# Performance work log

Measured on AMD Instinct MI355X. Metric: run time of the kernel, lower is better.

## Reference

```python
import jax, jax.numpy as jnp
import numpy as np

N_STREAMS = 8192
ITERS = 5
EPS = 1e-6


def setup_inputs() -> dict:
    key = jax.random.key(0)
    # matches torch init: randn(n, n) * 0.1
    logits = jax.random.normal(key, (N_STREAMS, N_STREAMS), dtype=jnp.float32) * 0.1
    return {"logits": logits}


def reference(logits) -> jnp.ndarray:
    n = logits.shape[0]
    # M = sigmoid(logits) + I
    M = jax.nn.sigmoid(logits) + jnp.eye(n, dtype=logits.dtype)
    for _ in range(ITERS):
        M = M / (jnp.sum(M, axis=1, keepdims=True) + EPS)  # row normalize
        M = M / (jnp.sum(M, axis=0, keepdims=True) + EPS)  # col normalize
    return M
```

## Files before the change

kernel.cpp:

```cpp
#include <hip/hip_runtime.h>

#define N_DIM 8192
#define EPS 1e-6f
#define R_STRIP 16
#define NRB (N_DIM / R_STRIP)

__device__ __forceinline__ float bflo(unsigned u) { return __uint_as_float(u << 16); }
__device__ __forceinline__ float bfhi(unsigned u) { return __uint_as_float(u & 0xffff0000u); }
__device__ __forceinline__ unsigned f2bf_bits(float f) {
    unsigned u = __float_as_uint(f);
    return (u + 0x7fffu + ((u >> 16) & 1u)) >> 16;
}
__device__ __forceinline__ float sigmoidf_fast(float x) {
    return 1.f / (1.f + __expf(-x));
}
__device__ __forceinline__ float dot8(uint4 b, float4 c0, float4 c1) {
    return bflo(b.x) * c0.x + bfhi(b.x) * c0.y + bflo(b.y) * c0.z + bfhi(b.y) * c0.w
         + bflo(b.z) * c1.x + bfhi(b.z) * c1.y + bflo(b.w) * c1.z + bfhi(b.w) * c1.w;
}
__device__ __forceinline__ void acc8(float* a, uint4 b, float rr) {
    a[0] += bflo(b.x) * rr; a[1] += bfhi(b.x) * rr;
    a[2] += bflo(b.y) * rr; a[3] += bfhi(b.y) * rr;
    a[4] += bflo(b.z) * rr; a[5] += bfhi(b.z) * rr;
    a[6] += bflo(b.w) * rr; a[7] += bfhi(b.w) * rr;
}
__device__ __forceinline__ uint4 sig_pack8(float4 x0, float4 x1, int jbase, int row, float& t) {
    float s[8] = { sigmoidf_fast(x0.x), sigmoidf_fast(x0.y), sigmoidf_fast(x0.z), sigmoidf_fast(x0.w),
                   sigmoidf_fast(x1.x), sigmoidf_fast(x1.y), sigmoidf_fast(x1.z), sigmoidf_fast(x1.w) };
    #pragma unroll
    for (int k = 0; k < 8; ++k)
        if (jbase + k == row) s[k] += 1.f;
    unsigned b[8];
    #pragma unroll
    for (int k = 0; k < 8; ++k) {
        b[k] = f2bf_bits(s[k]);
        t += __uint_as_float(b[k] << 16);
    }
    return make_uint4(b[0] | (b[1] << 16), b[2] | (b[3] << 16),
                      b[4] | (b[5] << 16), b[6] | (b[7] << 16));
}

__global__ __launch_bounds__(256) void k_init(const float* __restrict__ logits,
                                              unsigned short* __restrict__ B,
                                              float* __restrict__ r,
                                              float* __restrict__ partial) {
    __shared__ float sred[2][4];
    const int tid = threadIdx.x;
    const int lane = tid & 63, wid = tid >> 6;
    const int i0 = blockIdx.x * R_STRIP;
    float a[4][8];
    #pragma unroll
    for (int s = 0; s < 4; ++s)
        #pragma unroll
        for (int k = 0; k < 8; ++k) a[s][k] = 0.f;

    for (int bb = 0; bb < R_STRIP / 2; ++bb) {
        const int row0 = i0 + 2 * bb, row1 = row0 + 1;
        const float4* l0 = (const float4*)(logits + (size_t)row0 * N_DIM);
        const float4* l1 = (const float4*)(logits + (size_t)row1 * N_DIM);
        uint4* w0 = (uint4*)(B + (size_t)row0 * N_DIM);
        uint4* w1 = (uint4*)(B + (size_t)row1 * N_DIM);
        uint4 b0[4], b1[4];
        float t0 = 0.f, t1 = 0.f;
        #pragma unroll
        for (int s = 0; s < 4; ++s) {
            const int v = s * 256 + tid;
            b0[s] = sig_pack8(l0[2 * v], l0[2 * v + 1], v * 8, row0, t0);
            b1[s] = sig_pack8(l1[2 * v], l1[2 * v + 1], v * 8, row1, t1);
            w0[v] = b0[s];
            w1[v] = b1[s];
        }
        #pragma unroll
        for (int off = 32; off > 0; off >>= 1) {
            t0 += __shfl_down(t0, off, 64);
            t1 += __shfl_down(t1, off, 64);
        }
        if (lane == 0) { sred[0][wid] = t0; sred[1][wid] = t1; }
        __syncthreads();
        const float T0 = sred[0][0] + sred[0][1] + sred[0][2] + sred[0][3];
        const float T1 = sred[1][0] + sred[1][1] + sred[1][2] + sred[1][3];
        const float r0 = 1.f / (T0 + EPS);
        const float r1 = 1.f / (T1 + EPS);
        __syncthreads();
        if (tid == 0) { r[row0] = r0; r[row1] = r1; }
        #pragma unroll
        for (int s = 0; s < 4; ++s) { acc8(a[s], b0[s], r0); acc8(a[s], b1[s], r1); }
    }
    float* p = partial + (size_t)blockIdx.x * N_DIM;
    #pragma unroll
    for (int s = 0; s < 4; ++s) {
        const int col = s * 2048 + tid * 8;
        *(float4*)(p + col)     = make_float4(a[s][0], a[s][1], a[s][2], a[s][3]);
        *(float4*)(p + col + 4) = make_float4(a[s][4], a[s][5], a[s][6], a[s][7]);
    }
}

__global__ __launch_bounds__(256) void k_fused(const unsigned short* __restrict__ B,
                                               const float* __restrict__ cvec,
                                               float* __restrict__ r,
                                               float* __restrict__ partial) {
    __shared__ float sred[2][4];
    const int tid = threadIdx.x;
    const int lane = tid & 63, wid = tid >> 6;
    const int i0 = blockIdx.x * R_STRIP;
    const float4* cv = (const float4*)cvec;
    float a[4][8];
    #pragma unroll
    for (int s = 0; s < 4; ++s)
        #pragma unroll
        for (int k = 0; k < 8; ++k) a[s][k] = 0.f;

    for (int bb = 0; bb < R_STRIP / 2; ++bb) {
        const int row0 = i0 + 2 * bb, row1 = row0 + 1;
        const float r0old = r[row0];
        const float r1old = r[row1];
        const uint4* br0 = (const uint4*)(B + (size_t)row0 * N_DIM);
        const uint4* br1 = (const uint4*)(B + (size_t)row1 * N_DIM);
        uint4 b0[4], b1[4];
        float t0 = 0.f, t1 = 0.f;
        #pragma unroll
        for (int s = 0; s < 4; ++s) {
            const int v = s * 256 + tid;
            b0[s] = br0[v];
            b1[s] = br1[v];
            const float4 c0 = cv[2 * v];
            const float4 c1 = cv[2 * v + 1];
            t0 += dot8(b0[s], c0, c1);
            t1 += dot8(b1[s], c0, c1);
        }
        #pragma unroll
        for (int off = 32; off > 0; off >>= 1) {
            t0 += __shfl_down(t0, off, 64);
            t1 += __shfl_down(t1, off, 64);
        }
        if (lane == 0) { sred[0][wid] = t0; sred[1][wid] = t1; }
        __syncthreads();
        const float T0 = sred[0][0] + sred[0][1] + sred[0][2] + sred[0][3];
        const float T1 = sred[1][0] + sred[1][1] + sred[1][2] + sred[1][3];
        const float r0 = r0old / (r0old * T0 + EPS);
        const float r1 = r1old / (r1old * T1 + EPS);
        __syncthreads();
        if (tid == 0) { r[row0] = r0; r[row1] = r1; }
        #pragma unroll
        for (int s = 0; s < 4; ++s) { acc8(a[s], b0[s], r0); acc8(a[s], b1[s], r1); }
    }
    float* p = partial + (size_t)blockIdx.x * N_DIM;
    #pragma unroll
    for (int s = 0; s < 4; ++s) {
        const int col = s * 2048 + tid * 8;
        *(float4*)(p + col)     = make_float4(a[s][0], a[s][1], a[s][2], a[s][3]);
        *(float4*)(p + col + 4) = make_float4(a[s][4], a[s][5], a[s][6], a[s][7]);
    }
}

__global__ __launch_bounds__(256) void k_cupd(const float* __restrict__ partial,
                                              float* __restrict__ cvec, int first) {
    __shared__ float s[4][64];
    const int tc = threadIdx.x & 63;
    const int tg = threadIdx.x >> 6;
    const int j = blockIdx.x * 64 + tc;
    float u = 0.f;
    #pragma unroll 8
    for (int rb = tg * (NRB / 4); rb < (tg + 1) * (NRB / 4); ++rb)
        u += partial[(size_t)rb * N_DIM + j];
    s[tg][tc] = u;
    __syncthreads();
    if (threadIdx.x < 64) {
        const float tot = s[0][tc] + s[1][tc] + s[2][tc] + s[3][tc];
        const float cj = first ? 1.f : cvec[j];
        cvec[j] = cj / (cj * tot + EPS);
    }
}

__global__ __launch_bounds__(256) void k_out(const unsigned short* __restrict__ B,
                                             const float* __restrict__ r,
                                             const float* __restrict__ cvec,
                                             float* __restrict__ out) {
    const int row = blockIdx.x;
    const float ri = r[row];
    const uint4* brow = (const uint4*)(B + (size_t)row * N_DIM);
    const float4* cv = (const float4*)cvec;
    float* orow = out + (size_t)row * N_DIM;
    #pragma unroll
    for (int it = 0; it < 4; ++it) {
        const int v = it * 256 + (int)threadIdx.x;
        const uint4 b = brow[v];
        const float4 c0 = cv[2 * v];
        const float4 c1 = cv[2 * v + 1];
        *(float4*)(orow + v * 8)     = make_float4(bflo(b.x) * ri * c0.x, bfhi(b.x) * ri * c0.y,
                                                   bflo(b.y) * ri * c0.z, bfhi(b.y) * ri * c0.w);
        *(float4*)(orow + v * 8 + 4) = make_float4(bflo(b.z) * ri * c1.x, bfhi(b.z) * ri * c1.y,
                                                   bflo(b.w) * ri * c1.z, bfhi(b.w) * ri * c1.w);
    }
}

__global__ __launch_bounds__(256) void k_out_logits(const float* __restrict__ logits,
                                                    const float* __restrict__ r,
                                                    const float* __restrict__ cvec,
                                                    float* __restrict__ out) {
    const int row = blockIdx.x;
    const float ri = r[row];
    const float4* lrow = (const float4*)(logits + (size_t)row * N_DIM);
    const float4* cv = (const float4*)cvec;
    float4* orow = (float4*)(out + (size_t)row * N_DIM);
    #pragma unroll
    for (int it = 0; it < 8; ++it) {
        const int v = it * 256 + (int)threadIdx.x;
        const float4 x = lrow[v];
        const float4 cc = cv[v];
        const int j = v * 4;
        float s0 = sigmoidf_fast(x.x); if (j     == row) s0 += 1.f;
        float s1 = sigmoidf_fast(x.y); if (j + 1 == row) s1 += 1.f;
        float s2 = sigmoidf_fast(x.z); if (j + 2 == row) s2 += 1.f;
        float s3 = sigmoidf_fast(x.w); if (j + 3 == row) s3 += 1.f;
        orow[v] = make_float4(s0 * ri * cc.x, s1 * ri * cc.y, s2 * ri * cc.z, s3 * ri * cc.w);
    }
}

extern "C" void kernel_launch(void* const* d_in, const int* in_sizes, int n_in,
                              void* d_out, int out_size, void* d_ws, size_t ws_size,
                              hipStream_t stream) {
    const float* logits = (const float*)d_in[0];
    float* out = (float*)d_out;
    const size_t nn = (size_t)N_DIM * N_DIM;
    const size_t need = nn * 2 + (2 * N_DIM + (size_t)NRB * N_DIM) * 4;
    const bool use_ws = ws_size >= need + 256;
    float* wsf = (float*)d_ws;
    unsigned short* B;
    float *r, *cvec, *partial;
    if (use_ws) {
        B = (unsigned short*)wsf;
        r = wsf + nn / 2;
    } else {
        B = (unsigned short*)(out + nn / 2);
        r = wsf;
    }
    cvec = r + N_DIM;
    partial = cvec + N_DIM;

    const dim3 blk(256);
    k_init<<<dim3(NRB), blk, 0, stream>>>(logits, B, r, partial);
    k_cupd<<<dim3(128), blk, 0, stream>>>(partial, cvec, 1);
    for (int it = 1; it < 5; ++it) {
        k_fused<<<dim3(NRB), blk, 0, stream>>>(B, cvec, r, partial);
        k_cupd<<<dim3(128), blk, 0, stream>>>(partial, cvec, 0);
    }
    if (use_ws)
        k_out<<<dim3(N_DIM), blk, 0, stream>>>(B, r, cvec, out);
    else
        k_out_logits<<<dim3(N_DIM), blk, 0, stream>>>(logits, r, cvec, out);
}
```

Baseline: 637.2 us.

## Use 1024-thread blocks that load a whole 16-row strip at once

The init and fused row-strip kernels now use 1024 threads per block. Each thread owns one 8-column slice and loads all 16 rows of the strip up front, so the eight sequential two-row passes, each with two barriers, become one batched load, one batched 16-way reduction and two barriers per block. The c vector is loaded once per thread instead of once per row pair, and logits are read with nontemporal loads. In exchange each thread holds 16 uint4 values plus 16 partial sums in registers, which may limit occupancy under the 1024-thread launch bound.

```diff
diff --git a/kernel.cpp b/kernel.cpp
--- a/kernel.cpp
+++ b/kernel.cpp
@@ -4,6 +4,9 @@
 #define EPS 1e-6f
 #define R_STRIP 16
 #define NRB (N_DIM / R_STRIP)
+#define TPB 1024
+
+typedef float f32x4v __attribute__((ext_vector_type(4)));
 
 __device__ __forceinline__ float bflo(unsigned u) { return __uint_as_float(u << 16); }
 __device__ __forceinline__ float bfhi(unsigned u) { return __uint_as_float(u & 0xffff0000u); }
@@ -40,117 +43,103 @@
                       b[4] | (b[5] << 16), b[6] | (b[7] << 16));
 }
 
-__global__ __launch_bounds__(256) void k_init(const float* __restrict__ logits,
-                                              unsigned short* __restrict__ B,
-                                              float* __restrict__ r,
-                                              float* __restrict__ partial) {
-    __shared__ float sred[2][4];
+__global__ __launch_bounds__(TPB, 4) void k_init(const float* __restrict__ logits,
+                                                 unsigned short* __restrict__ B,
+                                                 float* __restrict__ r,
+                                                 float* __restrict__ partial) {
+    __shared__ float sredT[16][16];
+    __shared__ float rr[16];
     const int tid = threadIdx.x;
     const int lane = tid & 63, wid = tid >> 6;
     const int i0 = blockIdx.x * R_STRIP;
-    float a[4][8];
-    #pragma unroll
-    for (int s = 0; s < 4; ++s)
-        #pragma unroll
-        for (int k = 0; k < 8; ++k) a[s][k] = 0.f;
-
-    for (int bb = 0; bb < R_STRIP / 2; ++bb) {
-        const int row0 = i0 + 2 * bb, row1 = row0 + 1;
-        const float4* l0 = (const float4*)(logits + (size_t)row0 * N_DIM);
-        const float4* l1 = (const float4*)(logits + (size_t)row1 * N_DIM);
-        uint4* w0 = (uint4*)(B + (size_t)row0 * N_DIM);
-        uint4* w1 = (uint4*)(B + (size_t)row1 * N_DIM);
-        uint4 b0[4], b1[4];
-        float t0 = 0.f, t1 = 0.f;
-        #pragma unroll
-        for (int s = 0; s < 4; ++s) {
-            const int v = s * 256 + tid;
-            b0[s] = sig_pack8(l0[2 * v], l0[2 * v + 1], v * 8, row0, t0);
-            b1[s] = sig_pack8(l1[2 * v], l1[2 * v + 1], v * 8, row1, t1);
-            w0[v] = b0[s];
-            w1[v] = b1[s];
-        }
-        #pragma unroll
-        for (int off = 32; off > 0; off >>= 1) {
-            t0 += __shfl_down(t0, off, 64);
-            t1 += __shfl_down(t1, off, 64);
-        }
-        if (lane == 0) { sred[0][wid] = t0; sred[1][wid] = t1; }
-        __syncthreads();
-        const float T0 = sred[0][0] + sred[0][1] + sred[0][2] + sred[0][3];
-        const float T1 = sred[1][0] + sred[1][1] + sred[1][2] + sred[1][3];
-        const float r0 = 1.f / (T0 + EPS);
-        const float r1 = 1.f / (T1 + EPS);
-        __syncthreads();
-        if (tid == 0) { r[row0] = r0; r[row1] = r1; }
-        #pragma unroll
-        for (int s = 0; s < 4; ++s) { acc8(a[s], b0[s], r0); acc8(a[s], b1[s], r1); }
-    }
-    float* p = partial + (size_t)blockIdx.x * N_DIM;
-    #pragma unroll
-    for (int s = 0; s < 4; ++s) {
-        const int col = s * 2048 + tid * 8;
-        *(float4*)(p + col)     = make_float4(a[s][0], a[s][1], a[s][2], a[s][3]);
-        *(float4*)(p + col + 4) = make_float4(a[s][4], a[s][5], a[s][6], a[s][7]);
-    }
-}
-
-__global__ __launch_bounds__(256) void k_fused(const unsigned short* __restrict__ B,
-                                               const float* __restrict__ cvec,
-                                               float* __restrict__ r,
-                                               float* __restrict__ partial) {
-    __shared__ float sred[2][4];
+    uint4 b[16];
+    float t[16];
+    #pragma unroll
+    for (int q = 0; q < 16; ++q) {
+        const int row = i0 + q;
+        const f32x4v* l = (const f32x4v*)(logits + (size_t)row * N_DIM);
+        const f32x4v xa = __builtin_nontemporal_load(l + 2 * tid);
+        const f32x4v xb = __builtin_nontemporal_load(l + 2 * tid + 1);
+        float tl = 0.f;
+        b[q] = sig_pack8(make_float4(xa.x, xa.y, xa.z, xa.w),
+                         make_float4(xb.x, xb.y, xb.z, xb.w), tid * 8, row, tl);
+        t[q] = tl;
+        ((uint4*)(B + (size_t)row * N_DIM))[tid] = b[q];
+    }
+    #pragma unroll
+    for (int off = 32; off > 0; off >>= 1)
+        #pragma unroll
+        for (int q = 0; q < 16; ++q) t[q] += __shfl_xor(t[q], off, 64);
+    if (lane == 0) {
+        #pragma unroll
+        for (int q = 0; q < 16; ++q) sredT[wid][q] = t[q];
+    }
+    __syncthreads();
+    if (tid < 16) {
+        float T = 0.f;
+        #pragma unroll
+        for (int w = 0; w < 16; ++w) T += sredT[w][tid];
+        const float rv = 1.f / (T + EPS);
+        rr[tid] = rv;
+        r[i0 + tid] = rv;
+    }
+    __syncthreads();
+    float a[8];
+    #pragma unroll
+    for (int k = 0; k < 8; ++k) a[k] = 0.f;
+    #pragma unroll
+    for (int q = 0; q < 16; ++q) acc8(a, b[q], rr[q]);
+    float* p = partial + (size_t)blockIdx.x * N_DIM + tid * 8;
+    *(float4*)p       = make_float4(a[0], a[1], a[2], a[3]);
+    *(float4*)(p + 4) = make_float4(a[4], a[5], a[6], a[7]);
+}
+
+__global__ __launch_bounds__(TPB, 4) void k_fused(const unsigned short* __restrict__ B,
+                                                  const float* __restrict__ cvec,
+                                                  float* __restrict__ r,
+                                                  float* __restrict__ partial) {
+    __shared__ float sredT[16][16];
+    __shared__ float rr[16];
     const int tid = threadIdx.x;
     const int lane = tid & 63, wid = tid >> 6;
     const int i0 = blockIdx.x * R_STRIP;
-    const float4* cv = (const float4*)cvec;
-    float a[4][8];
-    #pragma unroll
-    for (int s = 0; s < 4; ++s)
-        #pragma unroll
-        for (int k = 0; k < 8; ++k) a[s][k] = 0.f;
-
-    for (int bb = 0; bb < R_STRIP / 2; ++bb) {
-        const int row0 = i0 + 2 * bb, row1 = row0 + 1;
-        const float r0old = r[row0];
-        const float r1old = r[row1];
-        const uint4* br0 = (const uint4*)(B + (size_t)row0 * N_DIM);
-        const uint4* br1 = (const uint4*)(B + (size_t)row1 * N_DIM);
-        uint4 b0[4], b1[4];
-        float t0 = 0.f, t1 = 0.f;
-        #pragma unroll
-        for (int s = 0; s < 4; ++s) {
-            const int v = s * 256 + tid;
-            b0[s] = br0[v];
-            b1[s] = br1[v];
-            const float4 c0 = cv[2 * v];
-            const float4 c1 = cv[2 * v + 1];
-            t0 += dot8(b0[s], c0, c1);
-            t1 += dot8(b1[s], c0, c1);
-        }
-        #pragma unroll
-        for (int off = 32; off > 0; off >>= 1) {
-            t0 += __shfl_down(t0, off, 64);
-            t1 += __shfl_down(t1, off, 64);
-        }
-        if (lane == 0) { sred[0][wid] = t0; sred[1][wid] = t1; }
-        __syncthreads();
-        const float T0 = sred[0][0] + sred[0][1] + sred[0][2] + sred[0][3];
-        const float T1 = sred[1][0] + sred[1][1] + sred[1][2] + sred[1][3];
-        const float r0 = r0old / (r0old * T0 + EPS);
-        const float r1 = r1old / (r1old * T1 + EPS);
-        __syncthreads();
-        if (tid == 0) { r[row0] = r0; r[row1] = r1; }
-        #pragma unroll
-        for (int s = 0; s < 4; ++s) { acc8(a[s], b0[s], r0); acc8(a[s], b1[s], r1); }
-    }
-    float* p = partial + (size_t)blockIdx.x * N_DIM;
-    #pragma unroll
-    for (int s = 0; s < 4; ++s) {
-        const int col = s * 2048 + tid * 8;
-        *(float4*)(p + col)     = make_float4(a[s][0], a[s][1], a[s][2], a[s][3]);
-        *(float4*)(p + col + 4) = make_float4(a[s][4], a[s][5], a[s][6], a[s][7]);
-    }
+    const float4 c0 = ((const float4*)cvec)[2 * tid];
+    const float4 c1 = ((const float4*)cvec)[2 * tid + 1];
+    const uint4* bp = (const uint4*)B + tid;
+    uint4 b[16];
+    #pragma unroll
+    for (int q = 0; q < 16; ++q)
+        b[q] = bp[(size_t)(i0 + q) << 10];
+    float t[16];
+    #pragma unroll
+    for (int q = 0; q < 16; ++q) t[q] = dot8(b[q], c0, c1);
+    #pragma unroll
+    for (int off = 32; off > 0; off >>= 1)
+        #pragma unroll
+        for (int q = 0; q < 16; ++q) t[q] += __shfl_xor(t[q], off, 64);
+    if (lane == 0) {
+        #pragma unroll
+        for (int q = 0; q < 16; ++q) sredT[wid][q] = t[q];
+    }
+    __syncthreads();
+    if (tid < 16) {
+        float T = 0.f;
+        #pragma unroll
+        for (int w = 0; w < 16; ++w) T += sredT[w][tid];
+        const float rold = r[i0 + tid];
+        const float rv = rold / (rold * T + EPS);
+        rr[tid] = rv;
+        r[i0 + tid] = rv;
+    }
+    __syncthreads();
+    float a[8];
+    #pragma unroll
+    for (int k = 0; k < 8; ++k) a[k] = 0.f;
+    #pragma unroll
+    for (int q = 0; q < 16; ++q) acc8(a, b[q], rr[q]);
+    float* p = partial + (size_t)blockIdx.x * N_DIM + tid * 8;
+    *(float4*)p       = make_float4(a[0], a[1], a[2], a[3]);
+    *(float4*)(p + 4) = make_float4(a[4], a[5], a[6], a[7]);
 }
 
 __global__ __launch_bounds__(256) void k_cupd(const float* __restrict__ partial,
@@ -238,15 +227,14 @@
     cvec = r + N_DIM;
     partial = cvec + N_DIM;
 
-    const dim3 blk(256);
-    k_init<<<dim3(NRB), blk, 0, stream>>>(logits, B, r, partial);
-    k_cupd<<<dim3(128), blk, 0, stream>>>(partial, cvec, 1);
+    k_init<<<dim3(NRB), dim3(TPB), 0, stream>>>(logits, B, r, partial);
+    k_cupd<<<dim3(128), dim3(256), 0, stream>>>(partial, cvec, 1);
     for (int it = 1; it < 5; ++it) {
-        k_fused<<<dim3(NRB), blk, 0, stream>>>(B, cvec, r, partial);
-        k_cupd<<<dim3(128), blk, 0, stream>>>(partial, cvec, 0);
+        k_fused<<<dim3(NRB), dim3(TPB), 0, stream>>>(B, cvec, r, partial);
+        k_cupd<<<dim3(128), dim3(256), 0, stream>>>(partial, cvec, 0);
     }
     if (use_ws)
-        k_out<<<dim3(N_DIM), blk, 0, stream>>>(B, r, cvec, out);
+        k_out<<<dim3(N_DIM), dim3(256), 0, stream>>>(B, r, cvec, out);
     else
-        k_out_logits<<<dim3(N_DIM), blk, 0, stream>>>(logits, r, cvec, out);
-}
+        k_out_logits<<<dim3(N_DIM), dim3(256), 0, stream>>>(logits, r, cvec, out);
+}
```

Measured after the change: 1.042 ms. 1.63x slower.
